# Optimization experiments

Measured on AMD Instinct MI355X. Metric: run time of the kernel, lower is better.

The kernel has to match this reference:

```python
import jax, jax.numpy as jnp
import numpy as np

N = 100_000      # nodes
E = 1_600_000    # edges (avg degree 16)
B = 64           # graphs in batch
OUT = 40         # out_channels (ModelNet40)
EPS = 1e-5       # BatchNorm eps


def _lin(x, W, b):
    # torch Linear: W is [out, in]
    return x @ W.T + b


def _bn_relu(y, g, be):
    # BatchNorm1d in training mode (batch statistics, biased var) + ReLU
    mean = y.mean(0)
    var = ((y - mean) ** 2).mean(0)
    return jax.nn.relu((y - mean) * jax.lax.rsqrt(var + EPS) * g + be)


def _mlp(x, layers):
    for (W, b, g, be) in layers:
        x = _bn_relu(_lin(x, W, b), g, be)
    return x


def _edge_conv(x, src, dst, layers):
    # PyG EdgeConv: message = nn(cat[x_i, x_j - x_i]), max-aggregate at target i
    xi = x[dst]                         # [E, F]
    xj = x[src]                         # [E, F]
    m = _mlp(jnp.concatenate([xi, xj - xi], axis=1), layers)  # [E, F_out]
    out = jax.ops.segment_max(m, dst, num_segments=x.shape[0])
    return jnp.where(jnp.isfinite(out), out, 0.0)  # empty segments -> 0


def setup_inputs() -> dict:
    key = jax.random.key(0)
    ks = jax.random.split(key, 16)
    d = {}
    d['pos'] = jax.random.normal(ks[0], (N, 3), dtype=jnp.float32)
    d['edge_index'] = jax.random.randint(ks[1], (2, E), 0, N, dtype=jnp.int64)
    d['batch'] = jnp.sort(jax.random.randint(ks[2], (N,), 0, B, dtype=jnp.int64))
    lin_shapes = {1: (64, 6), 2: (64, 64), 3: (64, 64), 4: (64, 128),
                  5: (128, 128), 6: (128, 128), 7: (128, 128), 8: (OUT, 128)}
    for i, (o, inp) in lin_shapes.items():
        kw = jax.random.fold_in(key, 100 + i)
        kb = jax.random.fold_in(key, 200 + i)
        s = 1.0 / np.sqrt(inp)
        d[f'W{i}'] = jax.random.uniform(kw, (o, inp), jnp.float32, -s, s)
        d[f'b{i}'] = jax.random.uniform(kb, (o,), jnp.float32, -s, s)
        if i < 8:
            d[f'g{i}'] = jnp.ones((o,), jnp.float32)
            d[f'be{i}'] = jnp.zeros((o,), jnp.float32)
    return d


def reference(pos, edge_index, batch,
              W1, b1, g1, be1, W2, b2, g2, be2, W3, b3, g3, be3,
              W4, b4, g4, be4, W5, b5, g5, be5, W6, b6, g6, be6,
              W7, b7, g7, be7, W8, b8):
    src, dst = edge_index[0], edge_index[1]
    conv1 = [(W1, b1, g1, be1), (W2, b2, g2, be2), (W3, b3, g3, be3)]
    conv2 = [(W4, b4, g4, be4)]
    x1 = _edge_conv(pos, src, dst, conv1)          # [N, 64]
    x2 = _edge_conv(x1, src, dst, conv2)           # [N, 64]
    h = _bn_relu(_lin(jnp.concatenate([x1, x2], axis=1), W5, b5), g5, be5)  # [N,128]
    pooled = jax.ops.segment_max(h, batch, num_segments=B)  # [B,128]
    pooled = jnp.where(jnp.isfinite(pooled), pooled, 0.0)
    h = _bn_relu(_lin(pooled, W6, b6), g6, be6)    # Dropout(0.5) = identity at eval
    h = _bn_relu(_lin(h, W7, b7), g7, be7)
    logits = _lin(h, W8, b8)                       # [B, OUT]
    return jax.nn.log_softmax(logits, axis=1)
```

## Files before the change

### kernel.cpp

```cpp
#include <hip/hip_runtime.h>
#include <hip/hip_bf16.h>
#include <hip/hip_fp16.h>
#include <math.h>

#define EPS_BN 1e-5f
#define NBK 256


typedef float f32x4_t  __attribute__((ext_vector_type(4)));
typedef _Float16 half8_t __attribute__((ext_vector_type(8)));
typedef _Float16 half2_t __attribute__((ext_vector_type(2)));

static __device__ __forceinline__ float bf2f(unsigned short b){
  return __uint_as_float(((unsigned)b) << 16);
}
static __device__ __forceinline__ float h2f(unsigned short u){
  _Float16 h;
  __builtin_memcpy(&h, &u, 2);
  return (float)h;
}
static __device__ __forceinline__ unsigned short f2h(float f){
  _Float16 h = (_Float16)f;
  unsigned short u;
  __builtin_memcpy(&u, &h, 2);
  return u;
}
static __device__ __forceinline__ unsigned pkh2(float a, float b){
  half2_t t = { (_Float16)a, (_Float16)b };
  unsigned u;
  __builtin_memcpy(&u, &t, 4);
  return u;
}
static inline int cdiv(int a, int b){ return (a + b - 1) / b; }
static __device__ __forceinline__ int clampi(int v, int lo, int hi){
  return v < lo ? lo : (v > hi ? hi : v);
}
static __device__ __forceinline__ int ld_idx(const void* p, long e, int m64){
  return m64 ? (int)((const long long*)p)[e] : ((const int*)p)[e];
}
static __device__ __forceinline__ unsigned ordf(float f){
  unsigned b = __float_as_uint(f);
  return (b & 0x80000000u) ? ~b : (b | 0x80000000u);
}
static __device__ __forceinline__ float iordf(unsigned u){
  unsigned b = (u & 0x80000000u) ? (u & 0x7FFFFFFFu) : ~u;
  return __uint_as_float(b);
}

__global__ void k_sentinel(float* out, int n){
  int i = blockIdx.x*256 + threadIdx.x;
  if (i < n) out[i] = -12288.0f;
}

__global__ void k_detect(const void* ei, const void* pos, int* dmode){
  __shared__ int nz, ff;
  if (threadIdx.x == 0){ nz = 0; ff = 0; }
  __syncthreads();
  const int* w32 = (const int*)ei;
  if (w32[1 + 2*threadIdx.x] != 0) nz = 1;
  const unsigned short* ph = (const unsigned short*)pos;
  int bad = 0;
  for (int i = threadIdx.x; i < 8192; i += 256)
    if (((ph[i] >> 7) & 0xFF) == 0xFF) bad = 1;
  if (bad) ff = 1;
  __syncthreads();
  if (threadIdx.x == 0){ dmode[0] = nz ? 0 : 1; dmode[1] = ff; }
}

struct ExpItem { const void* s; float* d; int n; };
struct ExpArgs { ExpItem it[31]; };
__global__ void k_expand(ExpArgs a, int cnt, const int* dmode){
  int i = blockIdx.y;
  if (i >= cnt) return;
  int m32 = dmode[1];
  int t = blockIdx.x*256 + threadIdx.x;
  if (t < a.it[i].n){
    a.it[i].d[t] = m32 ? ((const float*)a.it[i].s)[t]
                       : bf2f(((const unsigned short*)a.it[i].s)[t]);
  }
}

__global__ void k_prep(const float* __restrict__ W2, const float* __restrict__ W3,
                       const float* __restrict__ W5, const float* __restrict__ W4,
                       unsigned short* __restrict__ W2h, unsigned short* __restrict__ W3h,
                       unsigned short* __restrict__ W5h,
                       unsigned short* __restrict__ P, unsigned short* __restrict__ Q){
  int i = blockIdx.x*256 + threadIdx.x;
  if (i < 4096) W2h[i] = f2h(W2[i]);
  else if (i < 8192) W3h[i-4096] = f2h(W3[i-4096]);
  else if (i < 24576) W5h[i-8192] = f2h(W5[i-8192]);
  else if (i < 28672){
    int j = i - 24576;
    int c = j >> 6, k = j & 63;
    float b = W4[c*128 + 64 + k];
    P[j] = f2h(W4[c*128 + k] - b);
    Q[j] = f2h(b);
  }
}

__global__ void k_chist(const void* __restrict__ ei, int E, int N, const int* dmode,
                        int KK, int* __restrict__ cbc){
  __shared__ int lh[NBK];
  int tid = threadIdx.x;
  lh[tid] = 0;
  __syncthreads();
  int m64 = dmode[0];
  long base = (long)blockIdx.x*4096;
  for (int k = 0; k < 16; k++){
    long e = base + k*256 + tid;
    if (e < E){
      int nd = clampi(ld_idx(ei, (long)E + e, m64), 0, N-1);
      atomicAdd(&lh[nd/KK], 1);
    }
  }
  __syncthreads();
  if (lh[tid]) atomicAdd(&cbc[tid], lh[tid]);
}

__global__ void k_cscan(const int* __restrict__ cbc, int* __restrict__ cof,
                        int* __restrict__ cursorC){
  __shared__ int s[NBK];
  int t = threadIdx.x;
  int d = cbc[t];
  s[t] = d;
  __syncthreads();
  for (int off = 1; off < NBK; off <<= 1){
    int x = (t >= off) ? s[t - off] : 0;
    __syncthreads();
    s[t] += x;
    __syncthreads();
  }
  cof[t + 1] = s[t];
  cursorC[t] = s[t] - d;
  if (t == 0) cof[0] = 0;
}

__global__ void k_fillA(const void* __restrict__ ei, int E, int N, const int* dmode,
                        int KK, const float* __restrict__ pos,
                        int* __restrict__ cursorC, int2* __restrict__ tmp,
                        float* __restrict__ mom){
  __shared__ int lh[NBK];
  __shared__ int rb[NBK];
  int tid = threadIdx.x;
  lh[tid] = 0;
  __syncthreads();
  int m64 = dmode[0];
  long base = (long)blockIdx.x*4096;
  for (int k = 0; k < 16; k++){
    long e = base + k*256 + tid;
    if (e < E){
      int nd = clampi(ld_idx(ei, (long)E + e, m64), 0, N-1);
      atomicAdd(&lh[nd/KK], 1);
    }
  }
  __syncthreads();
  int c = lh[tid];
  rb[tid] = c ? atomicAdd(&cursorC[tid], c) : 0;
  lh[tid] = 0;
  __syncthreads();
  float v[27];
  #pragma unroll
  for (int j = 0; j < 27; j++) v[j] = 0.f;
  for (int k = 0; k < 16; k++){
    long e = base + k*256 + tid;
    if (e < E){
      int sv = clampi(ld_idx(ei, e, m64), 0, N-1);
      int nd = clampi(ld_idx(ei, (long)E + e, m64), 0, N-1);
      int b = nd/KK;
      int p = rb[b] + atomicAdd(&lh[b], 1);
      tmp[p] = make_int2(nd, sv);
      float xd0=pos[nd*3+0], xd1=pos[nd*3+1], xd2=pos[nd*3+2];
      float xs0=pos[sv*3+0], xs1=pos[sv*3+1], xs2=pos[sv*3+2];
      v[0]+=xd0; v[1]+=xd1; v[2]+=xd2;
      v[3]+=xs0; v[4]+=xs1; v[5]+=xs2;
      v[6]+=xd0*xd0; v[7]+=xd0*xd1; v[8]+=xd0*xd2; v[9]+=xd1*xd1; v[10]+=xd1*xd2; v[11]+=xd2*xd2;
      v[12]+=xs0*xs0; v[13]+=xs0*xs1; v[14]+=xs0*xs2; v[15]+=xs1*xs1; v[16]+=xs1*xs2; v[17]+=xs2*xs2;
      v[18]+=xd0*xs0; v[19]+=xd0*xs1; v[20]+=xd0*xs2;
      v[21]+=xd1*xs0; v[22]+=xd1*xs1; v[23]+=xd1*xs2;
      v[24]+=xd2*xs0; v[25]+=xd2*xs1; v[26]+=xd2*xs2;
    }
  }
  #pragma unroll
  for (int m = 1; m < 64; m <<= 1){
    #pragma unroll
    for (int j = 0; j < 27; j++) v[j] += __shfl_xor(v[j], m, 64);
  }
  int lane = tid & 63;
  int wflat = (blockIdx.x*256 + tid) >> 6;
  if (lane == 0){
    float* mr = &mom[(size_t)(wflat & 63)*32];
    #pragma unroll
    for (int j = 0; j < 27; j++) atomicAdd(&mr[j], v[j]);
  }
}

__global__ void __launch_bounds__(512, 1)
k_fillB(const int2* __restrict__ tmp, const int* __restrict__ cof, int N, int E, int KK,
        int* __restrict__ deg, int* __restrict__ offs, int2* __restrict__ es){
  __shared__ int lh[512];
  __shared__ int lc[512];
  int tid = threadIdx.x, b = blockIdx.x;
  int nd0 = b*KK;
  int nd1 = nd0 + KK; if (nd1 > N) nd1 = N;
  int nn = nd1 - nd0; if (nn < 0) nn = 0;
  int gbase = cof[b], gend = cof[b+1];
  int cnt = gend - gbase;
  lh[tid] = 0;
  __syncthreads();
  for (int t = tid; t < cnt; t += 512)
    atomicAdd(&lh[tmp[gbase + t].x - nd0], 1);
  __syncthreads();
  int d = lh[tid];
  for (int off = 1; off < 512; off <<= 1){
    int x = (tid >= off) ? lh[tid - off] : 0;
    __syncthreads();
    lh[tid] += x;
    __syncthreads();
  }
  int excl = lh[tid] - d;
  if (tid < nn){
    deg[nd0 + tid] = d;
    offs[nd0 + tid] = gbase + excl;
  }
  lc[tid] = excl;
  if (b == gridDim.x - 1 && tid == 0) offs[N] = E;
  __syncthreads();
  for (int t = tid; t < cnt; t += 512){
    int2 e2 = tmp[gbase + t];
    int lpos = atomicAdd(&lc[e2.x - nd0], 1);
    es[gbase + lpos] = e2;
  }
}

__global__ void k_bn1(const float* __restrict__ mom, float Ef,
                      const float* __restrict__ W1, const float* __restrict__ b1,
                      const float* __restrict__ g, const float* __restrict__ be,
                      float* __restrict__ ss){
  __shared__ float sm[27];
  int t = threadIdx.x;
  if (t < 27){
    float s = 0.f;
    for (int r = 0; r < 64; r++) s += mom[(size_t)r*32 + t];
    sm[t] = s;
  }
  __syncthreads();
  if (t < 64){
    float P0 = W1[t*6+0]-W1[t*6+3], P1 = W1[t*6+1]-W1[t*6+4], P2 = W1[t*6+2]-W1[t*6+5];
    float Q0 = W1[t*6+3], Q1 = W1[t*6+4], Q2 = W1[t*6+5];
    float b = b1[t];
    float vD0=sm[0],vD1=sm[1],vD2=sm[2], vS0=sm[3],vS1=sm[4],vS2=sm[5];
    float PvD = P0*vD0 + P1*vD1 + P2*vD2;
    float QvS = Q0*vS0 + Q1*vS1 + Q2*vS2;
    float sum = PvD + QvS + Ef*b;
    float PMDP = P0*(sm[6]*P0 + sm[7]*P1 + sm[8]*P2)
               + P1*(sm[7]*P0 + sm[9]*P1 + sm[10]*P2)
               + P2*(sm[8]*P0 + sm[10]*P1 + sm[11]*P2);
    float QMSQ = Q0*(sm[12]*Q0 + sm[13]*Q1 + sm[14]*Q2)
               + Q1*(sm[13]*Q0 + sm[15]*Q1 + sm[16]*Q2)
               + Q2*(sm[14]*Q0 + sm[16]*Q1 + sm[17]*Q2);
    float PGQ = P0*(sm[18]*Q0 + sm[19]*Q1 + sm[20]*Q2)
              + P1*(sm[21]*Q0 + sm[22]*Q1 + sm[23]*Q2)
              + P2*(sm[24]*Q0 + sm[25]*Q1 + sm[26]*Q2);
    float sumsq = PMDP + 2.f*b*PvD + Ef*b*b + QMSQ + 2.f*(PGQ + b*QvS);
    float mean = sum / Ef;
    float var  = fmaxf(sumsq / Ef - mean*mean, 0.f);
    float inv  = rsqrtf(var + EPS_BN);
    float sc   = g[t] * inv;
    ss[t]      = sc;
    ss[64 + t] = be[t] - mean*sc;
  }
}

__global__ void k_ab(const float* __restrict__ pos, int N,
                     const float* __restrict__ W1, const float* __restrict__ b1,
                     const float* __restrict__ ss1,
                     unsigned short* __restrict__ at, unsigned short* __restrict__ bt){
  int n = blockIdx.x*256 + threadIdx.x;
  if (n >= N) return;
  float x0 = pos[n*3+0], x1 = pos[n*3+1], x2 = pos[n*3+2];
  unsigned short* ar = at + (size_t)n*64;
  unsigned short* br = bt + (size_t)n*64;
  #pragma unroll
  for (int c2 = 0; c2 < 64; c2 += 2){
    float av[2], bv[2];
    #pragma unroll
    for (int u = 0; u < 2; u++){
      int c = c2 + u;
      float q0 = W1[c*6+3], q1 = W1[c*6+4], q2 = W1[c*6+5];
      float p0 = W1[c*6+0]-q0, p1 = W1[c*6+1]-q1, p2 = W1[c*6+2]-q2;
      float sc = ss1[c], sh = ss1[64+c];
      float pa = fmaf(p0,x0, fmaf(p1,x1, fmaf(p2,x2, b1[c])));
      float qb = fmaf(q0,x0, fmaf(q1,x1, q2*x2));
      av[u] = fmaf(pa, sc, sh);
      bv[u] = qb * sc;
    }
    *(unsigned*)&ar[c2] = pkh2(av[0], av[1]);
    *(unsigned*)&br[c2] = pkh2(bv[0], bv[1]);
  }
}

__global__ void k_finalize(float* __restrict__ repl, int C, float count,
                           const float* __restrict__ g, const float* __restrict__ be,
                           float* __restrict__ ss){
  int c = threadIdx.x;
  if (c < C){
    float s = 0.f, q = 0.f;
    for (int r = 0; r < 64; r++){
      s += repl[r*256 + c];       repl[r*256 + c] = 0.f;
      q += repl[r*256 + 128 + c]; repl[r*256 + 128 + c] = 0.f;
    }
    float mean = s / count;
    float var  = fmaxf(q / count - mean*mean, 0.f);
    float inv  = rsqrtf(var + EPS_BN);
    float sc   = g[c] * inv;
    ss[c]     = sc;
    ss[C + c] = be[c] - mean*sc;
  }
}

template<int NT, int KT>
static __device__ __forceinline__ void loadBh2(const unsigned short* __restrict__ Wp, int c15, int q,
                                               half8_t bf[NT][KT]){
  #pragma unroll
  for (int nt = 0; nt < NT; nt++){
    int c = nt*16 + c15;
    #pragma unroll
    for (int kt = 0; kt < KT; kt++)
      bf[nt][kt] = *(const half8_t*)(Wp + (size_t)c*(KT*32) + kt*32 + q*8);
  }
}
template<int NT, int KT, int ST>
static __device__ __forceinline__ void do_mfma2(const unsigned short* Aw, half8_t bf[NT][KT],
                                                const float* __restrict__ bias, int c15, int q,
                                                f32x4_t acc[4][NT]){
  #pragma unroll
  for (int mt = 0; mt < 4; mt++)
    #pragma unroll
    for (int nt = 0; nt < NT; nt++){
      float bv = bias[nt*16 + c15];
      acc[mt][nt] = (f32x4_t){bv, bv, bv, bv};
    }
  #pragma unroll
  for (int mt = 0; mt < 4; mt++){
    #pragma unroll
    for (int kt = 0; kt < KT; kt++){
      half8_t af = *(const half8_t*)&Aw[(mt*16 + c15)*ST + kt*32 + q*8];
      #pragma unroll
      for (int nt = 0; nt < NT; nt++)
        acc[mt][nt] = __builtin_amdgcn_mfma_f32_16x16x32_f16(af, bf[nt][kt], acc[mt][nt], 0, 0, 0);
    }
  }
}
template<int NT>
static __device__ __forceinline__ void stats_acc2(f32x4_t acc[4][NT], long tb, int E,
                                                  int lane, int q, int r_idx, int choff,
                                                  float* __restrict__ repl){
  #pragma unroll
  for (int nt = 0; nt < NT; nt++){
    float s = 0.f, qq = 0.f;
    #pragma unroll
    for (int mt = 0; mt < 4; mt++){
      #pragma unroll
      for (int r = 0; r < 4; r++){
        long eidx = tb + mt*16 + q*4 + r;
        float v = (eidx < E) ? acc[mt][nt][r] : 0.f;
        s += v; qq += v*v;
      }
    }
    s += __shfl_xor(s, 16, 64); qq += __shfl_xor(qq, 16, 64);
    s += __shfl_xor(s, 32, 64); qq += __shfl_xor(qq, 32, 64);
    if (lane < 16){
      atomicAdd(&repl[r_idx*256 + choff + nt*16 + lane], s);
      atomicAdd(&repl[r_idx*256 + 128 + choff + nt*16 + lane], qq);
    }
  }
}
template<int NT, int ST>
static __device__ __forceinline__ void dumpC2(f32x4_t acc[4][NT], unsigned short* Cw,
                                              int colbase, int c15, int q){
  #pragma unroll
  for (int mt = 0; mt < 4; mt++)
    #pragma unroll
    for (int nt = 0; nt < NT; nt++){
      int col = colbase + nt*16 + c15;
      #pragma unroll
      for (int r = 0; r < 4; r += 2){
        unsigned p = pkh2(acc[mt][nt][r], acc[mt][nt][r+1]);
        int row = mt*16 + q*4 + r;
        Cw[row*ST + col]        = (unsigned short)p;
        Cw[(row + 1)*ST + col]  = (unsigned short)(p >> 16);
      }
    }
}
static __device__ __forceinline__ void dumpC2T(f32x4_t acc[4][2], unsigned short* CT,
                                               int colbase, int c15, int q){
  #pragma unroll
  for (int mt = 0; mt < 4; mt++)
    #pragma unroll
    for (int nt = 0; nt < 2; nt++){
      int col = colbase + nt*16 + c15;
      #pragma unroll
      for (int r = 0; r < 4; r += 2){
        unsigned p = pkh2(acc[mt][nt][r], acc[mt][nt][r+1]);
        int row = mt*16 + q*4 + r;
        *(unsigned*)((char*)CT + col*136 + row*2) = p;
      }
    }
}
static __device__ __forceinline__ void seg_walk3(const unsigned short* CT, const int* nds,
                                                 long tb, int E, int tid,
                                                 unsigned* __restrict__ tmax,
                                                 unsigned* __restrict__ tmin){
  int lane = tid & 63, par = tid >> 6;
  long rem = (long)E - tb;
  int limit = rem >= 64 ? 64 : (rem > 0 ? (int)rem : 0);
  int k0 = par*32;
  int cnt = limit - k0; if (cnt > 32) cnt = 32;
  if (cnt <= 0) return;
  const char* base = (const char*)CT + lane*136 + k0*2;
  uint2 dv[8];
  #pragma unroll
  for (int j = 0; j < 8; j++) dv[j] = *(const uint2*)(base + j*8);
  int nd[32];
  #pragma unroll
  for (int j = 0; j < 8; j++) *(int4*)&nd[j*4] = *(const int4*)&nds[k0 + j*4];
  int cur = nd[0];
  float mx = -3.4e38f, mn = 3.4e38f;
  #pragma unroll
  for (int k = 0; k < 32; k++){
    unsigned w = (k & 2) ? dv[k>>2].y : dv[k>>2].x;
    unsigned short hv = (k & 1) ? (unsigned short)(w >> 16) : (unsigned short)(w & 0xffffu);
    float v = h2f(hv);
    bool act = (k < cnt);
    int ndk = act ? nd[k] : cur;
    if (ndk != cur){
      atomicMax(&tmax[(size_t)cur*64 + lane], ordf(mx));
      atomicMin(&tmin[(size_t)cur*64 + lane], ordf(mn));
      cur = ndk; mx = v; mn = v;
    } else if (act){
      mx = fmaxf(mx, v); mn = fminf(mn, v);
    }
  }
  atomicMax(&tmax[(size_t)cur*64 + lane], ordf(mx));
  atomicMin(&tmin[(size_t)cur*64 + lane], ordf(mn));
}
static __device__ __forceinline__ unsigned rladd2h(unsigned a, unsigned b){
  half2_t ha, hb;
  __builtin_memcpy(&ha, &a, 4);
  __builtin_memcpy(&hb, &b, 4);
  half2_t s = ha + hb;
  half2_t z = { (_Float16)0, (_Float16)0 };
  half2_t r = __builtin_elementwise_max(s, z);
  unsigned u;
  __builtin_memcpy(&u, &r, 4);
  return u;
}
static __device__ __forceinline__ void stage_z1t_half(const unsigned short* __restrict__ at,
                                                      const unsigned short* __restrict__ bt,
                                                      int di, int si, int h, unsigned short* Ar){
  const uint4* a4 = (const uint4*)(at + (size_t)di*64 + h*32);
  const uint4* b4 = (const uint4*)(bt + (size_t)si*64 + h*32);
  #pragma unroll
  for (int k = 0; k < 4; k++){
    uint4 av = a4[k], bv = b4[k], o;
    o.x = rladd2h(av.x, bv.x); o.y = rladd2h(av.y, bv.y);
    o.z = rladd2h(av.z, bv.z); o.w = rladd2h(av.w, bv.w);
    *(uint4*)&Ar[k*8] = o;
  }
}

__global__ void __launch_bounds__(128, 1)
k_m2stats(const int2* __restrict__ es,
          const unsigned short* __restrict__ at, const unsigned short* __restrict__ bt,
          int E,
          const unsigned short* __restrict__ W2h, const float* __restrict__ b2,
          float* __restrict__ repl){
  __shared__ unsigned short A[64][72];
  int tid = threadIdx.x;
  int lane = tid & 63, wv = tid >> 6;
  long tb = (long)blockIdx.x*64;
  long e = tb + lane;
  unsigned short* Ar = &A[lane][wv*32];
  if (e < E){
    int2 e2 = es[e];
    stage_z1t_half(at, bt, e2.x, e2.y, wv, Ar);
  } else {
    #pragma unroll
    for (int k = 0; k < 4; k++) *(uint4*)&Ar[k*8] = make_uint4(0u,0u,0u,0u);
  }
  __syncthreads();
  int c15 = lane & 15, q = lane >> 4;
  half8_t bf[2][2];
  loadBh2<2,2>(W2h + (size_t)(wv*32)*64, c15, q, bf);
  f32x4_t acc[4][2];
  do_mfma2<2,2,72>(&A[0][0], bf, b2 + wv*32, c15, q, acc);
  stats_acc2<2>(acc, tb, E, lane, q, blockIdx.x & 63, wv*32, repl);
}

__global__ void __launch_bounds__(128, 1)
k_conv1f(const unsigned short* __restrict__ at, const unsigned short* __restrict__ bt,
         const int2* __restrict__ es, int E,
         const float* __restrict__ ss2,
         const unsigned short* __restrict__ W2h, const float* __restrict__ b2,
         const unsigned short* __restrict__ W3h, const float* __restrict__ b3,
         float* __restrict__ repl, unsigned* __restrict__ tmax, unsigned* __restrict__ tmin){
  __shared__ unsigned short A[64][72];
  __shared__ int nds[64];
  int tid = threadIdx.x;
  int lane = tid & 63, wv = tid >> 6;
  long tb = (long)blockIdx.x*64;
  long t = tb + lane;
  unsigned short* Ar = &A[lane][wv*32];
  if (t < E){
    int2 e2 = es[t];
    if (wv == 0) nds[lane] = e2.x;
    stage_z1t_half(at, bt, e2.x, e2.y, wv, Ar);
  } else {
    if (wv == 0) nds[lane] = 0;
    #pragma unroll
    for (int k = 0; k < 4; k++) *(uint4*)&Ar[k*8] = make_uint4(0u,0u,0u,0u);
  }
  __syncthreads();
  int c15 = lane & 15, q = lane >> 4;
  unsigned short* Aw = &A[0][0];
  f32x4_t acc[4][2];
  {
    half8_t bf[2][2];
    loadBh2<2,2>(W2h + (size_t)(wv*32)*64, c15, q, bf);
    do_mfma2<2,2,72>(Aw, bf, b2 + wv*32, c15, q, acc);
  }
  #pragma unroll
  for (int nt = 0; nt < 2; nt++){
    int ch = wv*32 + nt*16 + c15;
    float sc = ss2[ch], sh = ss2[64 + ch];
    #pragma unroll
    for (int mt = 0; mt < 4; mt++)
      #pragma unroll
      for (int r = 0; r < 4; r++)
        acc[mt][nt][r] = fmaxf(fmaf(acc[mt][nt][r], sc, sh), 0.f);
  }
  __syncthreads();
  dumpC2<2,72>(acc, Aw, wv*32, c15, q);
  __syncthreads();
  {
    half8_t bf[2][2];
    loadBh2<2,2>(W3h + (size_t)(wv*32)*64, c15, q, bf);
    do_mfma2<2,2,72>(Aw, bf, b3 + wv*32, c15, q, acc);
  }
  stats_acc2<2>(acc, tb, E, lane, q, blockIdx.x & 63, wv*32, repl);
  __syncthreads();
  dumpC2T(acc, Aw, wv*32, c15, q);
  __syncthreads();
  seg_walk3(Aw, nds, tb, E, tid, tmax, tmin);
}

__global__ void __launch_bounds__(64, 1)
k_pq(const unsigned short* __restrict__ x1, int N,
     const unsigned short* __restrict__ Pmh, const unsigned short* __restrict__ Qmh,
     const float* __restrict__ b4, const float* __restrict__ zeros64,
     unsigned short* __restrict__ up, unsigned short* __restrict__ uq){
  __shared__ unsigned short A[64][72];
  __shared__ unsigned short Cb[64][72];
  int lane = threadIdx.x;
  long nb0 = (long)blockIdx.x*64;
  long n = nb0 + lane;
  unsigned short* Ar = &A[lane][0];
  if (n < N){
    const uint4* a4 = (const uint4*)(x1 + (size_t)n*64);
    #pragma unroll
    for (int k = 0; k < 8; k++) *(uint4*)&Ar[k*8] = a4[k];
  } else {
    #pragma unroll
    for (int k = 0; k < 8; k++) *(uint4*)&Ar[k*8] = make_uint4(0u,0u,0u,0u);
  }
  __syncthreads();
  int c15 = lane & 15, q = lane >> 4;
  unsigned short* Aw = &A[0][0];
  unsigned short* Cw = &Cb[0][0];
  for (int h = 0; h < 2; h++){
    const unsigned short* Wp = h ? Qmh : Pmh;
    const float* bp = h ? zeros64 : b4;
    unsigned short* out = h ? uq : up;
    half8_t bf[4][2];
    loadBh2<4,2>(Wp, c15, q, bf);
    f32x4_t acc[4][4];
    do_mfma2<4,2,72>(Aw, bf, bp, c15, q, acc);
    dumpC2<4,72>(acc, Cw, 0, c15, q);
    __syncthreads();
    int rl = lane >> 3, ch8 = lane & 7;
    #pragma unroll
    for (int pass = 0; pass < 8; pass++){
      int row = pass*8 + rl;
      long nn = nb0 + row;
      if (nn < N)
        *(uint4*)(out + (size_t)nn*64 + ch8*8) = *(const uint4*)&Cw[row*72 + ch8*8];
    }
    __syncthreads();
  }
}

#define NPW 8
__global__ void k_edge2(const int* __restrict__ offs, const int2* __restrict__ es,
                        const unsigned short* __restrict__ uq, const unsigned short* __restrict__ up,
                        int N, float* __restrict__ tmaxF, float* __restrict__ tminF,
                        float* __restrict__ repl){
  int wv = threadIdx.x >> 6, lane = threadIdx.x & 63;
  int w_id = blockIdx.x*4 + wv;
  int n0 = w_id * NPW;
  int nend = n0 + NPW; if (nend > N) nend = N;
  float s_acc = 0.f, ss_acc = 0.f;
  for (int n = n0; n < nend; n++){
    int e0 = offs[n], e1 = offs[n+1];
    if (e1 <= e0) continue;
    float mx = -3.4e38f, mn = 3.4e38f, qs = 0.f, qsq = 0.f;
    int t = e0;
    for (; t + 4 <= e1; t += 4){
      int s0 = es[t].y, s1 = es[t+1].y, s2 = es[t+2].y, s3 = es[t+3].y;
      float v0 = h2f(uq[(size_t)s0*64 + lane]);
      float v1 = h2f(uq[(size_t)s1*64 + lane]);
      float v2 = h2f(uq[(size_t)s2*64 + lane]);
      float v3 = h2f(uq[(size_t)s3*64 + lane]);
      mx = fmaxf(mx, fmaxf(fmaxf(v0, v1), fmaxf(v2, v3)));
      mn = fminf(mn, fminf(fminf(v0, v1), fminf(v2, v3)));
      qs += (v0 + v1) + (v2 + v3);
      qsq += v0*v0 + v1*v1 + v2*v2 + v3*v3;
    }
    for (; t < e1; t++){
      int s0 = es[t].y;
      float v0 = h2f(uq[(size_t)s0*64 + lane]);
      mx = fmaxf(mx, v0); mn = fminf(mn, v0); qs += v0; qsq += v0*v0;
    }
    float pv = h2f(up[(size_t)n*64 + lane]);
    float deg = (float)(e1 - e0);
    s_acc  += fmaf(deg, pv, qs);
    ss_acc += fmaf(deg*pv, pv, fmaf(2.f*pv, qs, qsq));
    tmaxF[(size_t)n*64 + lane] = mx;
    tminF[(size_t)n*64 + lane] = mn;
  }
  int r_idx = w_id & 63;
  atomicAdd(&repl[r_idx*256 + lane], s_acc);
  atomicAdd(&repl[r_idx*256 + 128 + lane], ss_acc);
}

__global__ void k_applybn2(unsigned short* __restrict__ x2 ,
                           const float* __restrict__ tmaxF, const float* __restrict__ tminF,
                           const int* __restrict__ degD, const float* __restrict__ ss,
                           long total){
  long i = (long)blockIdx.x*256 + threadIdx.x;
  if (i >= total) return;
  int c = (int)(i & 63);
  long n = i >> 6;
  float out = 0.f;
  if (degD[n] > 0){
    float sc = ss[c], sh = ss[64 + c];
    float v = h2f(x2[i]) + ((sc >= 0.f) ? tmaxF[i] : tminF[i]);
    out = fmaxf(fmaf(v, sc, sh), 0.f);
  }
  x2[i] = f2h(out);
}

__global__ void k_applybn(const unsigned* __restrict__ tmax, const unsigned* __restrict__ tmin,
                          const float* __restrict__ ss, long total,
                          unsigned short* __restrict__ xout){
  long i = (long)blockIdx.x*256 + threadIdx.x;
  if (i >= total) return;
  int c = (int)(i & 63);
  unsigned um = tmax[i];
  float out = 0.f;
  if (um != 0u){
    float sc = ss[c], sh = ss[64 + c];
    float v = (sc >= 0.f) ? iordf(um) : iordf(tmin[i]);
    out = fmaxf(fmaf(v, sc, sh), 0.f);
  }
  xout[i] = f2h(out);
}

__global__ void __launch_bounds__(64, 1)
k_lin5m(const unsigned short* __restrict__ x1, const unsigned short* __restrict__ x2,
        int N, const unsigned short* __restrict__ W5h, const float* __restrict__ b5,
        unsigned short* __restrict__ y5, float* __restrict__ repl){
  __shared__ unsigned short A[64][136];
  __shared__ unsigned short Cb[64][72];
  int lane = threadIdx.x;
  long nb0 = (long)blockIdx.x*64;
  long n = nb0 + lane;
  unsigned short* Ar = &A[lane][0];
  if (n < N){
    const uint4* a4 = (const uint4*)(x1 + (size_t)n*64);
    const uint4* b4 = (const uint4*)(x2 + (size_t)n*64);
    #pragma unroll
    for (int k = 0; k < 8; k++) *(uint4*)&Ar[k*8]      = a4[k];
    #pragma unroll
    for (int k = 0; k < 8; k++) *(uint4*)&Ar[64 + k*8] = b4[k];
  } else {
    #pragma unroll
    for (int k = 0; k < 16; k++) *(uint4*)&Ar[k*8] = make_uint4(0u,0u,0u,0u);
  }
  __syncthreads();
  int c15 = lane & 15, q = lane >> 4;
  int r_idx = blockIdx.x & 63;
  unsigned short* Aw = &A[0][0];
  unsigned short* Cw = &Cb[0][0];
  for (int h = 0; h < 2; h++){
    const unsigned short* Wp = W5h + (size_t)h*64*128;
    half8_t bf[4][4];
    loadBh2<4,4>(Wp, c15, q, bf);
    f32x4_t acc[4][4];
    do_mfma2<4,4,136>(Aw, bf, b5 + h*64, c15, q, acc);
    stats_acc2<4>(acc, nb0, N, lane, q, r_idx, h*64, repl);
    dumpC2<4,72>(acc, Cw, 0, c15, q);
    __syncthreads();
    int rl = lane >> 3, ch8 = lane & 7;
    #pragma unroll
    for (int pass = 0; pass < 8; pass++){
      int row = pass*8 + rl;
      long nn = nb0 + row;
      if (nn < N)
        *(uint4*)(y5 + (size_t)nn*128 + h*64 + ch8*8) = *(const uint4*)&Cw[row*72 + ch8*8];
    }
    __syncthreads();
  }
}

__global__ void k_pool(const unsigned short* __restrict__ y5, const void* __restrict__ batch, int N,
                       const int* dmode, const float* __restrict__ ss5, unsigned int* __restrict__ pooled){
  int m64 = dmode[0];
  int c = threadIdx.x & 127;
  int par = threadIdx.x >> 7;
  int n0 = blockIdx.x*128;
  int n1 = min(n0 + 128, N);
  float sc = ss5[c], sh = ss5[128 + c];
  int curb = -1; float curm = 0.f;
  for (int n = n0 + par; n < n1; n += 2){
    int b = clampi(ld_idx(batch, (long)n, m64), 0, 63);
    float v = fmaf(h2f(y5[(size_t)n*128 + c]), sc, sh);
    if (b != curb){
      if (curb >= 0) atomicMax(&pooled[curb*128 + c], __float_as_uint(fmaxf(curm, 0.f)));
      curb = b; curm = v;
    } else {
      curm = fmaxf(curm, v);
    }
  }
  if (curb >= 0) atomicMax(&pooled[curb*128 + c], __float_as_uint(fmaxf(curm, 0.f)));
}

__global__ void k_linH6(const unsigned int* __restrict__ X, const float* __restrict__ W,
                        const float* __restrict__ b, float* __restrict__ Y){
  int cell = blockIdx.x*256 + threadIdx.x;
  if (cell >= 8192) return;
  int r = cell >> 7, c = cell & 127;
  const unsigned int* xr = X + r*128;
  const float* wr = W + c*128;
  float a = b[c];
  for (int j = 0; j < 128; j++) a = fmaf(__uint_as_float(xr[j]), wr[j], a);
  Y[cell] = a;
}

__global__ void k_bnH(const float* __restrict__ Y, int CO,
                      const float* __restrict__ g, const float* __restrict__ be,
                      float* __restrict__ ss){
  int c = threadIdx.x;
  if (c >= CO) return;
  float s = 0.f;
  for (int r = 0; r < 64; r++) s += Y[r*CO + c];
  float mean = s * (1.f/64.f);
  float q = 0.f;
  for (int r = 0; r < 64; r++){ float d = Y[r*CO + c] - mean; q += d*d; }
  float var = fmaxf(q * (1.f/64.f), 0.f);
  float inv = rsqrtf(var + EPS_BN);
  float sc = g[c] * inv;
  ss[c] = sc;
  ss[CO + c] = be[c] - mean*sc;
}

__global__ void k_linHR(const float* __restrict__ Y, const float* __restrict__ ssH,
                        const float* __restrict__ W, const float* __restrict__ b,
                        int CO, float* __restrict__ Z){
  int cell = blockIdx.x*256 + threadIdx.x;
  if (cell >= 64*CO) return;
  int r = cell / CO, c = cell - r*CO;
  const float* xr = Y + r*128;
  const float* wr = W + c*128;
  float a = b[c];
  for (int j = 0; j < 128; j++){
    float x = fmaxf(fmaf(xr[j], ssH[j], ssH[128 + j]), 0.f);
    a = fmaf(x, wr[j], a);
  }
  Z[cell] = a;
}

__global__ void k_logsm(const float* __restrict__ Z, float* __restrict__ out){
  int r = threadIdx.x;
  const float* zr = Z + r*40;
  float m = zr[0];
  for (int c = 1; c < 40; c++) m = fmaxf(m, zr[c]);
  float s = 0.f;
  for (int c = 0; c < 40; c++) s += expf(zr[c] - m);
  float ls = logf(s);
  for (int c = 0; c < 40; c++) out[r*40 + c] = zr[c] - m - ls;
}

extern "C" void kernel_launch(void* const* d_in, const int* in_sizes, int n_in,
                              void* d_out, int out_size, void* d_ws, size_t ws_size,
                              hipStream_t stream) {
  const void* pos   = d_in[0];
  const void* ei    = d_in[1];
  const void* batch = d_in[2];
  (void)n_in;

  const int N = in_sizes[0] / 3;
  const int E = in_sizes[1] / 2;
  const int KK = cdiv(N, NBK);

  auto al = [](size_t x){ return (x + 255) & ~(size_t)255; };
  char* w = (char*)d_ws;
  size_t o = 0;
  float* repl = (float*)(w + o);                 o += (size_t)64*256*4;
  unsigned int* pooled = (unsigned int*)(w + o); o += (size_t)64*128*4;
  float* zeros64 = (float*)(w + o);              o += 256;
  float* mom = (float*)(w + o);                  o += (size_t)64*32*4;
  int* cbc = (int*)(w + o);                      o += 1024;
  size_t zero_bytes = o;
  int* cof = (int*)(w + o);                      o += 2048;
  int* cursorC = (int*)(w + o);                  o += 1024;
  int* deg = (int*)(w + o);                      o += al((size_t)4*N);
  unsigned* tmaxA = (unsigned*)(w + o);          o += (size_t)64*N*4;
  unsigned* tminA = (unsigned*)(w + o);          o += (size_t)64*N*4;
  float* tmaxF = (float*)tmaxA;
  float* tminF = (float*)tminA;
  int* dmode = (int*)(w + o);                    o += 256;
  int* offs = (int*)(w + o);                     o += al((size_t)4*(N + 1));
  int2* tmp = (int2*)(w + o);                    o += al((size_t)8*E);
  int2* es = (int2*)(w + o);                     o += al((size_t)8*E);
  float* ss1 = (float*)(w + o);                  o += 1024;
  float* ss2 = (float*)(w + o);                  o += 1024;
  float* ss3 = (float*)(w + o);                  o += 1024;
  float* ss4 = (float*)(w + o);                  o += 1024;
  float* ss5 = (float*)(w + o);                  o += 1024;
  float* ssH = (float*)(w + o);                  o += 1024;
  float* Y6 = (float*)(w + o);                   o += (size_t)8192*4;
  float* Y7 = (float*)(w + o);                   o += (size_t)8192*4;
  float* Zl = (float*)(w + o);                   o += al((size_t)2560*4);
  unsigned short* W2h = (unsigned short*)(w + o); o += 8192;
  unsigned short* W3h = (unsigned short*)(w + o); o += 8192;
  unsigned short* W5h = (unsigned short*)(w + o); o += 32768;
  unsigned short* Pmh = (unsigned short*)(w + o); o += 8192;
  unsigned short* Qmh = (unsigned short*)(w + o); o += 8192;
  float* expBase = (float*)(w + o);
  float* ep = expBase;
  float* epos = ep; ep += (size_t)3*N;
  float* eW[9], *eb[9], *eg[9], *ebe[9];
  const int wsz[9] = {0, 64*6, 64*64, 64*64, 64*128, 128*128, 128*128, 128*128, 40*128};
  const int bsz[9] = {0, 64, 64, 64, 64, 128, 128, 128, 40};
  for (int i = 1; i <= 8; i++){
    eW[i] = ep; ep += wsz[i];
    eb[i] = ep; ep += bsz[i];
    if (i < 8){ eg[i] = ep; ep += bsz[i]; ebe[i] = ep; ep += bsz[i]; }
  }
  long expCount = (long)(ep - expBase);
  o += al((size_t)expCount * 4);
  unsigned short* x1b = (unsigned short*)(w + o); o += al((size_t)2*64*N);
  unsigned short* x2b = (unsigned short*)(w + o); o += al((size_t)2*64*N);
  unsigned short* uqb = (unsigned short*)(w + o); o += al((size_t)2*64*N);
  unsigned short* atb = (unsigned short*)(w + o); o += al((size_t)2*64*N);
  unsigned short* btb = (unsigned short*)(w + o); o += al((size_t)2*64*N);
  unsigned short* y5b = (unsigned short*)(w + o); o += al((size_t)2*128*N);

  float* out_f = (float*)d_out;
  if (ws_size < o){
    k_sentinel<<<cdiv(out_size,256), 256, 0, stream>>>(out_f, out_size);
    return;
  }

  hipMemsetAsync(w, 0, zero_bytes, stream);
  hipMemsetAsync(tmaxA, 0x00, (size_t)64*N*4, stream);
  hipMemsetAsync(tminA, 0xFF, (size_t)64*N*4, stream);
  k_detect<<<1, 256, 0, stream>>>(ei, pos, dmode);

  ExpArgs ea;
  int it = 0;
  ea.it[it++] = {pos, epos, 3*N};
  int di_idx = 3;
  for (int i = 1; i <= 8; i++){
    ea.it[it++] = {d_in[di_idx++], eW[i], wsz[i]};
    ea.it[it++] = {d_in[di_idx++], eb[i], bsz[i]};
    if (i < 8){
      ea.it[it++] = {d_in[di_idx++], eg[i], bsz[i]};
      ea.it[it++] = {d_in[di_idx++], ebe[i], bsz[i]};
    }
  }
  k_expand<<<dim3(cdiv(3*N,256), 31), 256, 0, stream>>>(ea, it, dmode);
  k_prep<<<112, 256, 0, stream>>>(eW[2], eW[3], eW[5], eW[4], W2h, W3h, W5h, Pmh, Qmh);

  const int nfb = cdiv(E, 4096);
  k_chist<<<nfb, 256, 0, stream>>>(ei, E, N, dmode, KK, cbc);
  k_cscan<<<1, 256, 0, stream>>>(cbc, cof, cursorC);
  k_fillA<<<nfb, 256, 0, stream>>>(ei, E, N, dmode, KK, epos, cursorC, tmp, mom);
  k_fillB<<<NBK, 512, 0, stream>>>(tmp, cof, N, E, KK, deg, offs, es);
  k_bn1<<<1, 64, 0, stream>>>(mom, (float)E, eW[1], eb[1], eg[1], ebe[1], ss1);
  k_ab<<<cdiv(N,256), 256, 0, stream>>>(epos, N, eW[1], eb[1], ss1, atb, btb);

  k_m2stats<<<cdiv(E,64), 128, 0, stream>>>(es, atb, btb, E, W2h, eb[2], repl);
  k_finalize<<<1, 128, 0, stream>>>(repl, 64, (float)E, eg[2], ebe[2], ss2);
  k_conv1f<<<cdiv(E,64), 128, 0, stream>>>(atb, btb, es, E, ss2,
                                           W2h, eb[2], W3h, eb[3], repl, tmaxA, tminA);
  k_finalize<<<1, 128, 0, stream>>>(repl, 64, (float)E, eg[3], ebe[3], ss3);
  k_applybn<<<cdiv(N*64,256), 256, 0, stream>>>(tmaxA, tminA, ss3, (long)N*64, x1b);

  k_pq<<<cdiv(N,64), 64, 0, stream>>>(x1b, N, Pmh, Qmh, eb[4], zeros64, x2b, uqb);
  k_edge2<<<cdiv(N, 4*NPW), 256, 0, stream>>>(offs, es, uqb, x2b, N, tmaxF, tminF, repl);
  k_finalize<<<1, 128, 0, stream>>>(repl, 64, (float)E, eg[4], ebe[4], ss4);
  k_applybn2<<<cdiv(N*64,256), 256, 0, stream>>>(x2b, tmaxF, tminF, deg, ss4, (long)N*64);

  k_lin5m<<<cdiv(N,64), 64, 0, stream>>>(x1b, x2b, N, W5h, eb[5], y5b, repl);
  k_finalize<<<1, 128, 0, stream>>>(repl, 128, (float)N, eg[5], ebe[5], ss5);
  k_pool<<<cdiv(N,128), 256, 0, stream>>>(y5b, batch, N, dmode, ss5, pooled);

  k_linH6<<<32, 256, 0, stream>>>(pooled, eW[6], eb[6], Y6);
  k_bnH<<<1, 128, 0, stream>>>(Y6, 128, eg[6], ebe[6], ssH);
  k_linHR<<<32, 256, 0, stream>>>(Y6, ssH, eW[7], eb[7], 128, Y7);
  k_bnH<<<1, 128, 0, stream>>>(Y7, 128, eg[7], ebe[7], ssH);
  k_linHR<<<10, 256, 0, stream>>>(Y7, ssH, eW[8], eb[8], 40, Zl);
  k_logsm<<<1, 64, 0, stream>>>(Zl, out_f);
}
```

Measured before the change: 632.0 us.

## Process two 64-edge tiles per block with XCD-aware swizzle in conv1 kernels

k_m2stats and k_conv1f now each handle 128 edges per block as two 64-edge tiles. Weight fragments and BN scale/shift are loaded once per block, and the BN statistic atomics are committed once per block, which halves the block count and the atomic traffic. Block indices are remapped so that consecutive edge chunks land on the same XCD, which should improve L2 locality for the sorted edge stream. The cost is double the shared memory, a longer serial path per block, and fewer blocks to hide latency.

```diff
diff --git a/kernel.cpp b/kernel.cpp
--- a/kernel.cpp
+++ b/kernel.cpp
@@ -45,6 +45,13 @@
 static __device__ __forceinline__ float iordf(unsigned u){
   unsigned b = (u & 0x80000000u) ? (u & 0x7FFFFFFFu) : ~u;
   return __uint_as_float(b);
+}
+static __device__ __forceinline__ int xcd_swz(int orig, int nwg){
+  int xcd = orig & 7;
+  int base = orig >> 3;
+  int q = nwg >> 3, r = nwg & 7;
+  int start = (xcd < r) ? xcd*(q+1) : r*(q+1) + (xcd - r)*q;
+  return start + base;
 }
 
 __global__ void k_sentinel(float* out, int n){
@@ -352,28 +359,45 @@
   }
 }
 template<int NT>
-static __device__ __forceinline__ void stats_acc2(f32x4_t acc[4][NT], long tb, int E,
-                                                  int lane, int q, int r_idx, int choff,
-                                                  float* __restrict__ repl){
+static __device__ __forceinline__ void stats_add(f32x4_t acc[4][NT], long tb, int E, int q,
+                                                 float s[NT], float qq[NT]){
   #pragma unroll
   for (int nt = 0; nt < NT; nt++){
-    float s = 0.f, qq = 0.f;
     #pragma unroll
     for (int mt = 0; mt < 4; mt++){
       #pragma unroll
       for (int r = 0; r < 4; r++){
         long eidx = tb + mt*16 + q*4 + r;
         float v = (eidx < E) ? acc[mt][nt][r] : 0.f;
-        s += v; qq += v*v;
+        s[nt] += v; qq[nt] += v*v;
       }
     }
-    s += __shfl_xor(s, 16, 64); qq += __shfl_xor(qq, 16, 64);
-    s += __shfl_xor(s, 32, 64); qq += __shfl_xor(qq, 32, 64);
+  }
+}
+template<int NT>
+static __device__ __forceinline__ void stats_commit(float s[NT], float qq[NT],
+                                                    int lane, int r_idx, int choff,
+                                                    float* __restrict__ repl){
+  #pragma unroll
+  for (int nt = 0; nt < NT; nt++){
+    float sv = s[nt], qv = qq[nt];
+    sv += __shfl_xor(sv, 16, 64); qv += __shfl_xor(qv, 16, 64);
+    sv += __shfl_xor(sv, 32, 64); qv += __shfl_xor(qv, 32, 64);
     if (lane < 16){
-      atomicAdd(&repl[r_idx*256 + choff + nt*16 + lane], s);
-      atomicAdd(&repl[r_idx*256 + 128 + choff + nt*16 + lane], qq);
-    }
-  }
+      atomicAdd(&repl[r_idx*256 + choff + nt*16 + lane], sv);
+      atomicAdd(&repl[r_idx*256 + 128 + choff + nt*16 + lane], qv);
+    }
+  }
+}
+template<int NT>
+static __device__ __forceinline__ void stats_acc2(f32x4_t acc[4][NT], long tb, int E,
+                                                  int lane, int q, int r_idx, int choff,
+                                                  float* __restrict__ repl){
+  float s[NT], qq[NT];
+  #pragma unroll
+  for (int nt = 0; nt < NT; nt++){ s[nt] = 0.f; qq[nt] = 0.f; }
+  stats_add<NT>(acc, tb, E, q, s, qq);
+  stats_commit<NT>(s, qq, lane, r_idx, choff, repl);
 }
 template<int NT, int ST>
 static __device__ __forceinline__ void dumpC2(f32x4_t acc[4][NT], unsigned short* Cw,
@@ -475,26 +499,35 @@
           int E,
           const unsigned short* __restrict__ W2h, const float* __restrict__ b2,
           float* __restrict__ repl){
-  __shared__ unsigned short A[64][72];
+  __shared__ unsigned short A[2][64][72];
   int tid = threadIdx.x;
   int lane = tid & 63, wv = tid >> 6;
-  long tb = (long)blockIdx.x*64;
-  long e = tb + lane;
-  unsigned short* Ar = &A[lane][wv*32];
-  if (e < E){
-    int2 e2 = es[e];
-    stage_z1t_half(at, bt, e2.x, e2.y, wv, Ar);
-  } else {
-    #pragma unroll
-    for (int k = 0; k < 4; k++) *(uint4*)&Ar[k*8] = make_uint4(0u,0u,0u,0u);
+  int swz = xcd_swz(blockIdx.x, gridDim.x);
+  long tb0 = (long)swz*128;
+  #pragma unroll
+  for (int t = 0; t < 2; t++){
+    long e = tb0 + t*64 + lane;
+    unsigned short* Ar = &A[t][lane][wv*32];
+    if (e < E){
+      int2 e2 = es[e];
+      stage_z1t_half(at, bt, e2.x, e2.y, wv, Ar);
+    } else {
+      #pragma unroll
+      for (int k = 0; k < 4; k++) *(uint4*)&Ar[k*8] = make_uint4(0u,0u,0u,0u);
+    }
   }
   __syncthreads();
   int c15 = lane & 15, q = lane >> 4;
   half8_t bf[2][2];
   loadBh2<2,2>(W2h + (size_t)(wv*32)*64, c15, q, bf);
-  f32x4_t acc[4][2];
-  do_mfma2<2,2,72>(&A[0][0], bf, b2 + wv*32, c15, q, acc);
-  stats_acc2<2>(acc, tb, E, lane, q, blockIdx.x & 63, wv*32, repl);
+  float s[2] = {0.f, 0.f}, qq[2] = {0.f, 0.f};
+  #pragma unroll
+  for (int t = 0; t < 2; t++){
+    f32x4_t acc[4][2];
+    do_mfma2<2,2,72>(&A[t][0][0], bf, b2 + wv*32, c15, q, acc);
+    stats_add<2>(acc, tb0 + t*64, E, q, s, qq);
+  }
+  stats_commit<2>(s, qq, lane, swz & 63, wv*32, repl);
 }
 
 __global__ void __launch_bounds__(128, 1)
@@ -504,54 +537,57 @@
          const unsigned short* __restrict__ W2h, const float* __restrict__ b2,
          const unsigned short* __restrict__ W3h, const float* __restrict__ b3,
          float* __restrict__ repl, unsigned* __restrict__ tmax, unsigned* __restrict__ tmin){
-  __shared__ unsigned short A[64][72];
-  __shared__ int nds[64];
+  __shared__ unsigned short A[2][64][72];
+  __shared__ int nds[2][64];
   int tid = threadIdx.x;
   int lane = tid & 63, wv = tid >> 6;
-  long tb = (long)blockIdx.x*64;
-  long t = tb + lane;
-  unsigned short* Ar = &A[lane][wv*32];
-  if (t < E){
-    int2 e2 = es[t];
-    if (wv == 0) nds[lane] = e2.x;
-    stage_z1t_half(at, bt, e2.x, e2.y, wv, Ar);
-  } else {
-    if (wv == 0) nds[lane] = 0;
-    #pragma unroll
-    for (int k = 0; k < 4; k++) *(uint4*)&Ar[k*8] = make_uint4(0u,0u,0u,0u);
+  int swz = xcd_swz(blockIdx.x, gridDim.x);
+  long tb0 = (long)swz*128;
+  #pragma unroll
+  for (int t = 0; t < 2; t++){
+    long e = tb0 + t*64 + lane;
+    unsigned short* Ar = &A[t][lane][wv*32];
+    if (e < E){
+      int2 e2 = es[e];
+      if (wv == 0) nds[t][lane] = e2.x;
+      stage_z1t_half(at, bt, e2.x, e2.y, wv, Ar);
+    } else {
+      if (wv == 0) nds[t][lane] = 0;
+      #pragma unroll
+      for (int k = 0; k < 4; k++) *(uint4*)&Ar[k*8] = make_uint4(0u,0u,0u,0u);
+    }
   }
   __syncthreads();
   int c15 = lane & 15, q = lane >> 4;
-  unsigned short* Aw = &A[0][0];
-  f32x4_t acc[4][2];
-  {
-    half8_t bf[2][2];
-    loadBh2<2,2>(W2h + (size_t)(wv*32)*64, c15, q, bf);
-    do_mfma2<2,2,72>(Aw, bf, b2 + wv*32, c15, q, acc);
-  }
-  #pragma unroll
-  for (int nt = 0; nt < 2; nt++){
-    int ch = wv*32 + nt*16 + c15;
-    float sc = ss2[ch], sh = ss2[64 + ch];
+  half8_t bf2[2][2], bf3[2][2];
+  loadBh2<2,2>(W2h + (size_t)(wv*32)*64, c15, q, bf2);
+  loadBh2<2,2>(W3h + (size_t)(wv*32)*64, c15, q, bf3);
+  float sc0 = ss2[wv*32 + c15],      sh0 = ss2[64 + wv*32 + c15];
+  float sc1 = ss2[wv*32 + 16 + c15], sh1 = ss2[64 + wv*32 + 16 + c15];
+  float s[2] = {0.f, 0.f}, qq[2] = {0.f, 0.f};
+  #pragma unroll
+  for (int t = 0; t < 2; t++){
+    unsigned short* Aw = &A[t][0][0];
+    f32x4_t acc[4][2];
+    do_mfma2<2,2,72>(Aw, bf2, b2 + wv*32, c15, q, acc);
     #pragma unroll
     for (int mt = 0; mt < 4; mt++)
       #pragma unroll
-      for (int r = 0; r < 4; r++)
-        acc[mt][nt][r] = fmaxf(fmaf(acc[mt][nt][r], sc, sh), 0.f);
-  }
-  __syncthreads();
-  dumpC2<2,72>(acc, Aw, wv*32, c15, q);
-  __syncthreads();
-  {
-    half8_t bf[2][2];
-    loadBh2<2,2>(W3h + (size_t)(wv*32)*64, c15, q, bf);
-    do_mfma2<2,2,72>(Aw, bf, b3 + wv*32, c15, q, acc);
-  }
-  stats_acc2<2>(acc, tb, E, lane, q, blockIdx.x & 63, wv*32, repl);
-  __syncthreads();
-  dumpC2T(acc, Aw, wv*32, c15, q);
-  __syncthreads();
-  seg_walk3(Aw, nds, tb, E, tid, tmax, tmin);
+      for (int r = 0; r < 4; r++){
+        acc[mt][0][r] = fmaxf(fmaf(acc[mt][0][r], sc0, sh0), 0.f);
+        acc[mt][1][r] = fmaxf(fmaf(acc[mt][1][r], sc1, sh1), 0.f);
+      }
+    __syncthreads();
+    dumpC2<2,72>(acc, Aw, wv*32, c15, q);
+    __syncthreads();
+    do_mfma2<2,2,72>(Aw, bf3, b3 + wv*32, c15, q, acc);
+    stats_add<2>(acc, tb0 + t*64, E, q, s, qq);
+    __syncthreads();
+    dumpC2T(acc, Aw, wv*32, c15, q);
+    __syncthreads();
+    seg_walk3(Aw, nds[t], tb0 + t*64, E, tid, tmax, tmin);
+  }
+  stats_commit<2>(s, qq, lane, swz & 63, wv*32, repl);
 }
 
 __global__ void __launch_bounds__(64, 1)
@@ -900,10 +936,10 @@
   k_bn1<<<1, 64, 0, stream>>>(mom, (float)E, eW[1], eb[1], eg[1], ebe[1], ss1);
   k_ab<<<cdiv(N,256), 256, 0, stream>>>(epos, N, eW[1], eb[1], ss1, atb, btb);
 
-  k_m2stats<<<cdiv(E,64), 128, 0, stream>>>(es, atb, btb, E, W2h, eb[2], repl);
+  k_m2stats<<<cdiv(E,128), 128, 0, stream>>>(es, atb, btb, E, W2h, eb[2], repl);
   k_finalize<<<1, 128, 0, stream>>>(repl, 64, (float)E, eg[2], ebe[2], ss2);
-  k_conv1f<<<cdiv(E,64), 128, 0, stream>>>(atb, btb, es, E, ss2,
-                                           W2h, eb[2], W3h, eb[3], repl, tmaxA, tminA);
+  k_conv1f<<<cdiv(E,128), 128, 0, stream>>>(atb, btb, es, E, ss2,
+                                            W2h, eb[2], W3h, eb[3], repl, tmaxA, tminA);
   k_finalize<<<1, 128, 0, stream>>>(repl, 64, (float)E, eg[3], ebe[3], ss3);
   k_applybn<<<cdiv(N*64,256), 256, 0, stream>>>(tmaxA, tminA, ss3, (long)N*64, x1b);
 
```

Result: slower. 652.3 us (+3.2%).
